# Kernel tuning notes

Measured on AMD Instinct MI355X. Metric: run time of the kernel, lower is better.

Reference implementation:

```python
import jax, jax.numpy as jnp
import numpy as np

B, T, I, H, O = 4096, 256, 16, 32, 1


def setup_inputs() -> dict:
    key = jax.random.key(0)
    ks = jax.random.split(key, 8)
    s_ih = 1.0 / np.sqrt(H)
    x = jax.random.normal(ks[0], (B, T, I), dtype=jnp.float32)
    # PyTorch nn.LSTM params: gate order [i, f, g, o], uniform(-1/sqrt(H), 1/sqrt(H))
    W_ih = jax.random.uniform(ks[1], (4 * H, I), minval=-s_ih, maxval=s_ih, dtype=jnp.float32)
    W_hh = jax.random.uniform(ks[2], (4 * H, H), minval=-s_ih, maxval=s_ih, dtype=jnp.float32)
    b_ih = jax.random.uniform(ks[3], (4 * H,), minval=-s_ih, maxval=s_ih, dtype=jnp.float32)
    b_hh = jax.random.uniform(ks[4], (4 * H,), minval=-s_ih, maxval=s_ih, dtype=jnp.float32)
    W_fc = jax.random.uniform(ks[5], (O, H), minval=-s_ih, maxval=s_ih, dtype=jnp.float32)
    b_fc = jax.random.uniform(ks[6], (O,), minval=-s_ih, maxval=s_ih, dtype=jnp.float32)
    return {"x": x, "W_ih": W_ih, "W_hh": W_hh, "b_ih": b_ih, "b_hh": b_hh,
            "W_fc": W_fc, "b_fc": b_fc}


def _lstm_last_hidden(x, W_ih, W_hh, b_ih, b_hh):
    # Precompute input contributions for all timesteps: [T, B, 4H]
    xg = (jnp.einsum('bti,gi->btg', x, W_ih) + b_ih + b_hh).transpose(1, 0, 2)
    h0 = jnp.zeros((x.shape[0], W_hh.shape[1]), dtype=x.dtype)
    c0 = jnp.zeros_like(h0)

    def step(carry, xg_t):
        h, c = carry
        gates = xg_t + h @ W_hh.T  # [B, 4H]
        i, f, g, o = jnp.split(gates, 4, axis=-1)
        i = jax.nn.sigmoid(i)
        f = jax.nn.sigmoid(f)
        g = jnp.tanh(g)
        o = jax.nn.sigmoid(o)
        c = f * c + i * g
        h = o * jnp.tanh(c)
        return (h, c), None

    (h_last, _), _ = jax.lax.scan(step, (h0, c0), xg)
    return h_last


def reference(x, W_ih, W_hh, b_ih, b_hh, W_fc, b_fc):
    h_last = _lstm_last_hidden(x, W_ih, W_hh, b_ih, b_hh)
    # Dropout is identity in eval mode
    return h_last @ W_fc.T + b_fc  # [B, O]
```

## Files before the change

kernel.cpp:

```cpp
#include <hip/hip_runtime.h>

#define B_ 4096
#define T_ 256
#define I_ 16
#define H_ 32

typedef _Float16 half2_t __attribute__((ext_vector_type(2)));
typedef _Float16 half4_t __attribute__((ext_vector_type(4)));
typedef _Float16 half8_t __attribute__((ext_vector_type(8)));

union H8 {
    half8_t v;
    half2_t h[4];
};

__device__ __forceinline__ float sigm_(float x) {
    float e = __builtin_amdgcn_exp2f(-1.442695041f * x);
    return __builtin_amdgcn_rcpf(1.0f + e);
}
__device__ __forceinline__ float tanh_(float x) {
    float e = __builtin_amdgcn_exp2f(-2.885390082f * x);
    float r = __builtin_amdgcn_rcpf(1.0f + e);
    return __fmaf_rn(2.0f, r, -1.0f);
}

__global__ __launch_bounds__(64, 4)
void lstm_fused_f16(const float* __restrict__ x,
                    const float* __restrict__ Wih,
                    const float* __restrict__ Whh,
                    const float* __restrict__ bih,
                    const float* __restrict__ bhh,
                    const float* __restrict__ Wfc,
                    const float* __restrict__ bfc,
                    float* __restrict__ out)
{
    __shared__ __align__(16) _Float16 hbuf[2][H_];
    __shared__ __align__(16) _Float16 xbuf[2][8 * I_];

    const int tid  = threadIdx.x;
    const int elem = tid >> 5;
    const int idx  = tid & 31;
    const int b    = blockIdx.x * 2 + elem;

    half2_t wih2[4][I_ / 2];
    half2_t whh2[4][H_ / 2];
    float bias[4];
#pragma unroll
    for (int q = 0; q < 4; ++q) {
        const int row = q * 32 + idx;
        const float4* pih = reinterpret_cast<const float4*>(Wih + row * I_);
#pragma unroll
        for (int k = 0; k < I_ / 4; ++k) {
            const float4 v = pih[k];
            wih2[q][2 * k + 0] = half2_t{(_Float16)v.x, (_Float16)v.y};
            wih2[q][2 * k + 1] = half2_t{(_Float16)v.z, (_Float16)v.w};
        }
        const float4* phh = reinterpret_cast<const float4*>(Whh + row * H_);
#pragma unroll
        for (int k = 0; k < H_ / 4; ++k) {
            const float4 v = phh[k];
            whh2[q][2 * k + 0] = half2_t{(_Float16)v.x, (_Float16)v.y};
            whh2[q][2 * k + 1] = half2_t{(_Float16)v.z, (_Float16)v.w};
        }
        bias[q] = bih[row] + bhh[row];
    }

    hbuf[elem][idx] = (_Float16)0.0f;
    float c  = 0.0f;
    float hj = 0.0f;
    __syncthreads();

    const float* xb = x + (size_t)b * (T_ * I_);
    float4 xnext = *reinterpret_cast<const float4*>(xb + idx * 4);

    for (int tb = 0; tb < T_ / 8; ++tb) {
        half4_t xs;
        xs[0] = (_Float16)xnext.x; xs[1] = (_Float16)xnext.y;
        xs[2] = (_Float16)xnext.z; xs[3] = (_Float16)xnext.w;
        *reinterpret_cast<half4_t*>(&xbuf[elem][idx * 4]) = xs;
        if (tb + 1 < T_ / 8) {
            xnext = *reinterpret_cast<const float4*>(xb + (tb + 1) * (8 * I_) + idx * 4);
        }
        __syncthreads();

#pragma unroll
        for (int tt = 0; tt < 8; ++tt) {
            float ai = bias[0], af = bias[1], ag = bias[2], ao = bias[3];

            H8 xv0, xv1;
            xv0.v = *reinterpret_cast<const half8_t*>(&xbuf[elem][tt * I_]);
            xv1.v = *reinterpret_cast<const half8_t*>(&xbuf[elem][tt * I_ + 8]);
#pragma unroll
            for (int k = 0; k < 4; ++k) {
                ai = __builtin_amdgcn_fdot2(xv0.h[k], wih2[0][k], ai, false);
                af = __builtin_amdgcn_fdot2(xv0.h[k], wih2[1][k], af, false);
                ag = __builtin_amdgcn_fdot2(xv0.h[k], wih2[2][k], ag, false);
                ao = __builtin_amdgcn_fdot2(xv0.h[k], wih2[3][k], ao, false);
            }
#pragma unroll
            for (int k = 0; k < 4; ++k) {
                ai = __builtin_amdgcn_fdot2(xv1.h[k], wih2[0][4 + k], ai, false);
                af = __builtin_amdgcn_fdot2(xv1.h[k], wih2[1][4 + k], af, false);
                ag = __builtin_amdgcn_fdot2(xv1.h[k], wih2[2][4 + k], ag, false);
                ao = __builtin_amdgcn_fdot2(xv1.h[k], wih2[3][4 + k], ao, false);
            }

#pragma unroll
            for (int j8 = 0; j8 < 4; ++j8) {
                H8 hv;
                hv.v = *reinterpret_cast<const half8_t*>(&hbuf[elem][j8 * 8]);
#pragma unroll
                for (int k = 0; k < 4; ++k) {
                    const int p = j8 * 4 + k;
                    ai = __builtin_amdgcn_fdot2(hv.h[k], whh2[0][p], ai, false);
                    af = __builtin_amdgcn_fdot2(hv.h[k], whh2[1][p], af, false);
                    ag = __builtin_amdgcn_fdot2(hv.h[k], whh2[2][p], ag, false);
                    ao = __builtin_amdgcn_fdot2(hv.h[k], whh2[3][p], ao, false);
                }
            }

            const float gi = sigm_(ai);
            const float gf = sigm_(af);
            const float gg = tanh_(ag);
            const float go = sigm_(ao);

            c  = __fmaf_rn(gf, c, gi * gg);
            hj = go * tanh_(c);

            hbuf[elem][idx] = (_Float16)hj;
            __syncthreads();
        }
    }

    float p = hj * Wfc[idx];
#pragma unroll
    for (int off = 16; off > 0; off >>= 1) {
        p += __shfl_down(p, off, 32);
    }
    if (idx == 0) {
        out[b] = p + bfc[0];
    }
}

extern "C" void kernel_launch(void* const* d_in, const int* in_sizes, int n_in,
                              void* d_out, int out_size, void* d_ws, size_t ws_size,
                              hipStream_t stream) {
    const float* x   = (const float*)d_in[0];
    const float* Wih = (const float*)d_in[1];
    const float* Whh = (const float*)d_in[2];
    const float* bih = (const float*)d_in[3];
    const float* bhh = (const float*)d_in[4];
    const float* Wfc = (const float*)d_in[5];
    const float* bfc = (const float*)d_in[6];
    float* out = (float*)d_out;

    dim3 grid(B_ / 2);
    dim3 block(64);
    hipLaunchKernelGGL(lstm_fused_f16, grid, block, 0, stream,
                       x, Wih, Whh, bih, bhh, Wfc, bfc, out);
}
```

Before: 239.6 us.

## Split LSTM gates across two half-waves, one batch element per block

Each 64-thread block now handles one batch element instead of two. Each lane computes two gate rows (i/g in the low half, f/o in the high half), and results are exchanged with a cross-half shuffle. This halves the per-step dot-product chain length per lane and uses two accumulators per row for more ILP, which targets the serial recurrence latency. In exchange it doubles the number of blocks, idles half the lanes for the cell update, and doubles the x staging chunk to 16 timesteps.

```diff
diff --git a/kernel.cpp b/kernel.cpp
--- a/kernel.cpp
+++ b/kernel.cpp
@@ -25,119 +25,126 @@
 }
 
 __global__ __launch_bounds__(64, 4)
-void lstm_fused_f16(const float* __restrict__ x,
-                    const float* __restrict__ Wih,
-                    const float* __restrict__ Whh,
-                    const float* __restrict__ bih,
-                    const float* __restrict__ bhh,
-                    const float* __restrict__ Wfc,
-                    const float* __restrict__ bfc,
-                    float* __restrict__ out)
+void lstm_gate_split(const float* __restrict__ x,
+                     const float* __restrict__ Wih,
+                     const float* __restrict__ Whh,
+                     const float* __restrict__ bih,
+                     const float* __restrict__ bhh,
+                     const float* __restrict__ Wfc,
+                     const float* __restrict__ bfc,
+                     float* __restrict__ out)
 {
-    __shared__ __align__(16) _Float16 hbuf[2][H_];
-    __shared__ __align__(16) _Float16 xbuf[2][8 * I_];
+    __shared__ __align__(16) _Float16 hbuf[H_];
+    __shared__ __align__(16) _Float16 xbuf[16 * I_];
 
     const int tid  = threadIdx.x;
-    const int elem = tid >> 5;
-    const int idx  = tid & 31;
-    const int b    = blockIdx.x * 2 + elem;
+    const int b    = blockIdx.x;
+    const bool lo  = (tid < 32);
 
-    half2_t wih2[4][I_ / 2];
-    half2_t whh2[4][H_ / 2];
-    float bias[4];
+    const int rowA = tid;
+    const int rowB = tid + 64;
+
+    half2_t wA[24], wB[24];
 #pragma unroll
-    for (int q = 0; q < 4; ++q) {
-        const int row = q * 32 + idx;
-        const float4* pih = reinterpret_cast<const float4*>(Wih + row * I_);
+    for (int k = 0; k < I_ / 4; ++k) {
+        const float4 va = *reinterpret_cast<const float4*>(Wih + rowA * I_ + 4 * k);
+        wA[2 * k + 0] = half2_t{(_Float16)va.x, (_Float16)va.y};
+        wA[2 * k + 1] = half2_t{(_Float16)va.z, (_Float16)va.w};
+        const float4 vb = *reinterpret_cast<const float4*>(Wih + rowB * I_ + 4 * k);
+        wB[2 * k + 0] = half2_t{(_Float16)vb.x, (_Float16)vb.y};
+        wB[2 * k + 1] = half2_t{(_Float16)vb.z, (_Float16)vb.w};
+    }
 #pragma unroll
-        for (int k = 0; k < I_ / 4; ++k) {
-            const float4 v = pih[k];
-            wih2[q][2 * k + 0] = half2_t{(_Float16)v.x, (_Float16)v.y};
-            wih2[q][2 * k + 1] = half2_t{(_Float16)v.z, (_Float16)v.w};
-        }
-        const float4* phh = reinterpret_cast<const float4*>(Whh + row * H_);
-#pragma unroll
-        for (int k = 0; k < H_ / 4; ++k) {
-            const float4 v = phh[k];
-            whh2[q][2 * k + 0] = half2_t{(_Float16)v.x, (_Float16)v.y};
-            whh2[q][2 * k + 1] = half2_t{(_Float16)v.z, (_Float16)v.w};
-        }
-        bias[q] = bih[row] + bhh[row];
+    for (int k = 0; k < H_ / 4; ++k) {
+        const float4 va = *reinterpret_cast<const float4*>(Whh + rowA * H_ + 4 * k);
+        wA[8 + 2 * k + 0] = half2_t{(_Float16)va.x, (_Float16)va.y};
+        wA[8 + 2 * k + 1] = half2_t{(_Float16)va.z, (_Float16)va.w};
+        const float4 vb = *reinterpret_cast<const float4*>(Whh + rowB * H_ + 4 * k);
+        wB[8 + 2 * k + 0] = half2_t{(_Float16)vb.x, (_Float16)vb.y};
+        wB[8 + 2 * k + 1] = half2_t{(_Float16)vb.z, (_Float16)vb.w};
     }
+    const float biasA = bih[rowA] + bhh[rowA];
+    const float biasB = bih[rowB] + bhh[rowB];
 
-    hbuf[elem][idx] = (_Float16)0.0f;
+    const float mB   = lo ? -2.885390082f : -1.442695041f;
+    const float mulB = lo ? 2.0f : 1.0f;
+    const float addB = lo ? -1.0f : 0.0f;
+
+    if (lo) hbuf[tid] = (_Float16)0.0f;
     float c  = 0.0f;
     float hj = 0.0f;
     __syncthreads();
 
     const float* xb = x + (size_t)b * (T_ * I_);
-    float4 xnext = *reinterpret_cast<const float4*>(xb + idx * 4);
+    float4 xnext = *reinterpret_cast<const float4*>(xb + tid * 4);
 
-    for (int tb = 0; tb < T_ / 8; ++tb) {
+    for (int tb = 0; tb < T_ / 16; ++tb) {
         half4_t xs;
         xs[0] = (_Float16)xnext.x; xs[1] = (_Float16)xnext.y;
         xs[2] = (_Float16)xnext.z; xs[3] = (_Float16)xnext.w;
-        *reinterpret_cast<half4_t*>(&xbuf[elem][idx * 4]) = xs;
-        if (tb + 1 < T_ / 8) {
-            xnext = *reinterpret_cast<const float4*>(xb + (tb + 1) * (8 * I_) + idx * 4);
+        *reinterpret_cast<half4_t*>(&xbuf[tid * 4]) = xs;
+        if (tb + 1 < T_ / 16) {
+            xnext = *reinterpret_cast<const float4*>(xb + (tb + 1) * (16 * I_) + tid * 4);
         }
         __syncthreads();
 
 #pragma unroll
-        for (int tt = 0; tt < 8; ++tt) {
-            float ai = bias[0], af = bias[1], ag = bias[2], ao = bias[3];
+        for (int tt = 0; tt < 16; ++tt) {
+            float aA0 = biasA, aA1 = 0.0f, aB0 = biasB, aB1 = 0.0f;
 
             H8 xv0, xv1;
-            xv0.v = *reinterpret_cast<const half8_t*>(&xbuf[elem][tt * I_]);
-            xv1.v = *reinterpret_cast<const half8_t*>(&xbuf[elem][tt * I_ + 8]);
+            xv0.v = *reinterpret_cast<const half8_t*>(&xbuf[tt * I_]);
+            xv1.v = *reinterpret_cast<const half8_t*>(&xbuf[tt * I_ + 8]);
 #pragma unroll
             for (int k = 0; k < 4; ++k) {
-                ai = __builtin_amdgcn_fdot2(xv0.h[k], wih2[0][k], ai, false);
-                af = __builtin_amdgcn_fdot2(xv0.h[k], wih2[1][k], af, false);
-                ag = __builtin_amdgcn_fdot2(xv0.h[k], wih2[2][k], ag, false);
-                ao = __builtin_amdgcn_fdot2(xv0.h[k], wih2[3][k], ao, false);
+                aA0 = __builtin_amdgcn_fdot2(xv0.h[k], wA[k], aA0, false);
+                aB0 = __builtin_amdgcn_fdot2(xv0.h[k], wB[k], aB0, false);
+                aA1 = __builtin_amdgcn_fdot2(xv1.h[k], wA[4 + k], aA1, false);
+                aB1 = __builtin_amdgcn_fdot2(xv1.h[k], wB[4 + k], aB1, false);
             }
-#pragma unroll
-            for (int k = 0; k < 4; ++k) {
-                ai = __builtin_amdgcn_fdot2(xv1.h[k], wih2[0][4 + k], ai, false);
-                af = __builtin_amdgcn_fdot2(xv1.h[k], wih2[1][4 + k], af, false);
-                ag = __builtin_amdgcn_fdot2(xv1.h[k], wih2[2][4 + k], ag, false);
-                ao = __builtin_amdgcn_fdot2(xv1.h[k], wih2[3][4 + k], ao, false);
-            }
-
 #pragma unroll
             for (int j8 = 0; j8 < 4; ++j8) {
                 H8 hv;
-                hv.v = *reinterpret_cast<const half8_t*>(&hbuf[elem][j8 * 8]);
+                hv.v = *reinterpret_cast<const half8_t*>(&hbuf[j8 * 8]);
 #pragma unroll
                 for (int k = 0; k < 4; ++k) {
-                    const int p = j8 * 4 + k;
-                    ai = __builtin_amdgcn_fdot2(hv.h[k], whh2[0][p], ai, false);
-                    af = __builtin_amdgcn_fdot2(hv.h[k], whh2[1][p], af, false);
-                    ag = __builtin_amdgcn_fdot2(hv.h[k], whh2[2][p], ag, false);
-                    ao = __builtin_amdgcn_fdot2(hv.h[k], whh2[3][p], ao, false);
+                    const int p = 8 + j8 * 4 + k;
+                    if (j8 & 1) {
+                        aA1 = __builtin_amdgcn_fdot2(hv.h[k], wA[p], aA1, false);
+                        aB1 = __builtin_amdgcn_fdot2(hv.h[k], wB[p], aB1, false);
+                    } else {
+                        aA0 = __builtin_amdgcn_fdot2(hv.h[k], wA[p], aA0, false);
+                        aB0 = __builtin_amdgcn_fdot2(hv.h[k], wB[p], aB0, false);
+                    }
                 }
             }
+            const float aA = aA0 + aA1;
+            const float aB = aB0 + aB1;
 
-            const float gi = sigm_(ai);
-            const float gf = sigm_(af);
-            const float gg = tanh_(ag);
-            const float go = sigm_(ao);
+            const float actA = sigm_(aA);
+            const float eB   = __builtin_amdgcn_exp2f(mB * aB);
+            const float sB   = __builtin_amdgcn_rcpf(1.0f + eB);
+            const float actB = __fmaf_rn(mulB, sB, addB);
 
-            c  = __fmaf_rn(gf, c, gi * gg);
-            hj = go * tanh_(c);
+            const float xA = __shfl_xor(actA, 32, 64);
+            const float xB = __shfl_xor(actB, 32, 64);
 
-            hbuf[elem][idx] = (_Float16)hj;
+            if (lo) {
+                c = __fmaf_rn(xA, c, actA * actB);
+                const float tc = tanh_(c);
+                hj = xB * tc;
+                hbuf[tid] = (_Float16)hj;
+            }
             __syncthreads();
         }
     }
 
-    float p = hj * Wfc[idx];
+    float p = lo ? hj * Wfc[tid] : 0.0f;
 #pragma unroll
-    for (int off = 16; off > 0; off >>= 1) {
-        p += __shfl_down(p, off, 32);
+    for (int off = 32; off > 0; off >>= 1) {
+        p += __shfl_down(p, off, 64);
     }
-    if (idx == 0) {
+    if (tid == 0) {
         out[b] = p + bfc[0];
     }
 }
@@ -154,8 +161,8 @@
     const float* bfc = (const float*)d_in[6];
     float* out = (float*)d_out;
 
-    dim3 grid(B_ / 2);
+    dim3 grid(B_);
     dim3 block(64);
-    hipLaunchKernelGGL(lstm_fused_f16, grid, block, 0, stream,
+    hipLaunchKernelGGL(lstm_gate_split, grid, block, 0, stream,
                        x, Wih, Whh, bih, bhh, Wfc, bfc, out);
 }
```

Result: slower. 254.2 us (+6.1%).

## Compute LSTM gates with MFMA over 16 batch elements per block

Applied to the files above, without the earlier changes.

Replaces the per-thread fdot2 gate computation with 16x16x32 f16 MFMA instructions. Each 128-thread block handles 16 sequences, and each wave computes half of the hidden units for all four gates. The input projection becomes a zero-padded MFMA, the bias is pre-scaled and folded into the activation exponent, x is prefetched one 8-step block ahead in registers, and h is double-buffered in LDS. This reduces the ALU work per timestep, but the grid drops to 256 blocks, which may underfill the GPU and leave the serial recurrence latency-bound.

```diff
diff --git a/kernel.cpp b/kernel.cpp
--- a/kernel.cpp
+++ b/kernel.cpp
@@ -5,140 +5,139 @@
 #define I_ 16
 #define H_ 32
 
-typedef _Float16 half2_t __attribute__((ext_vector_type(2)));
-typedef _Float16 half4_t __attribute__((ext_vector_type(4)));
-typedef _Float16 half8_t __attribute__((ext_vector_type(8)));
+typedef _Float16 f16x4 __attribute__((ext_vector_type(4)));
+typedef _Float16 f16x8 __attribute__((ext_vector_type(8)));
+typedef float    f32x4 __attribute__((ext_vector_type(4)));
 
-union H8 {
-    half8_t v;
-    half2_t h[4];
-};
+#define MSIG  (-1.442695041f)
+#define MTANH (-2.885390082f)
 
-__device__ __forceinline__ float sigm_(float x) {
-    float e = __builtin_amdgcn_exp2f(-1.442695041f * x);
-    return __builtin_amdgcn_rcpf(1.0f + e);
-}
-__device__ __forceinline__ float tanh_(float x) {
-    float e = __builtin_amdgcn_exp2f(-2.885390082f * x);
-    float r = __builtin_amdgcn_rcpf(1.0f + e);
-    return __fmaf_rn(2.0f, r, -1.0f);
-}
-
-__global__ __launch_bounds__(64, 4)
-void lstm_fused_f16(const float* __restrict__ x,
-                    const float* __restrict__ Wih,
-                    const float* __restrict__ Whh,
-                    const float* __restrict__ bih,
-                    const float* __restrict__ bhh,
-                    const float* __restrict__ Wfc,
-                    const float* __restrict__ bfc,
-                    float* __restrict__ out)
+__global__ __launch_bounds__(128, 1)
+void lstm_mfma2(const float* __restrict__ x,
+                const float* __restrict__ Wih,
+                const float* __restrict__ Whh,
+                const float* __restrict__ bih,
+                const float* __restrict__ bhh,
+                const float* __restrict__ Wfc,
+                const float* __restrict__ bfc,
+                float* __restrict__ out)
 {
-    __shared__ __align__(16) _Float16 hbuf[2][H_];
-    __shared__ __align__(16) _Float16 xbuf[2][8 * I_];
+    __shared__ __align__(16) _Float16 hbuf[2][16][40];
 
     const int tid  = threadIdx.x;
-    const int elem = tid >> 5;
-    const int idx  = tid & 31;
-    const int b    = blockIdx.x * 2 + elem;
+    const int wave = tid >> 6;
+    const int l    = tid & 63;
+    const int lr   = l & 15;
+    const int lg   = l >> 4;
+    const int b0   = blockIdx.x * 16;
 
-    half2_t wih2[4][I_ / 2];
-    half2_t whh2[4][H_ / 2];
-    float bias[4];
+    f16x8 whhA[4];
+    f16x8 wihA[4];
+    float mb[4][4];
 #pragma unroll
     for (int q = 0; q < 4; ++q) {
-        const int row = q * 32 + idx;
-        const float4* pih = reinterpret_cast<const float4*>(Wih + row * I_);
+        const int rowA = q * 32 + wave * 16 + lr;
+        const float* ph = Whh + rowA * H_ + lg * 8;
 #pragma unroll
-        for (int k = 0; k < I_ / 4; ++k) {
-            const float4 v = pih[k];
-            wih2[q][2 * k + 0] = half2_t{(_Float16)v.x, (_Float16)v.y};
-            wih2[q][2 * k + 1] = half2_t{(_Float16)v.z, (_Float16)v.w};
+        for (int k = 0; k < 8; ++k) whhA[q][k] = (_Float16)ph[k];
+        const float* pi = Wih + rowA * I_ + (lg & 1) * 8;
+#pragma unroll
+        for (int k = 0; k < 8; ++k)
+            wihA[q][k] = (lg < 2) ? (_Float16)pi[k] : (_Float16)0.0f;
+        const float m = (q == 2) ? MTANH : MSIG;
+#pragma unroll
+        for (int r = 0; r < 4; ++r) {
+            const int rowC = q * 32 + wave * 16 + lg * 4 + r;
+            mb[q][r] = m * (bih[rowC] + bhh[rowC]);
         }
-        const float4* phh = reinterpret_cast<const float4*>(Whh + row * H_);
-#pragma unroll
-        for (int k = 0; k < H_ / 4; ++k) {
-            const float4 v = phh[k];
-            whh2[q][2 * k + 0] = half2_t{(_Float16)v.x, (_Float16)v.y};
-            whh2[q][2 * k + 1] = half2_t{(_Float16)v.z, (_Float16)v.w};
-        }
-        bias[q] = bih[row] + bhh[row];
     }
 
-    hbuf[elem][idx] = (_Float16)0.0f;
-    float c  = 0.0f;
-    float hj = 0.0f;
+    for (int i = tid; i < 2 * 16 * 40; i += 128)
+        ((_Float16*)hbuf)[i] = (_Float16)0.0f;
     __syncthreads();
 
-    const float* xb = x + (size_t)b * (T_ * I_);
-    float4 xnext = *reinterpret_cast<const float4*>(xb + idx * 4);
+    float c0 = 0.f, c1 = 0.f, c2 = 0.f, c3 = 0.f;
 
-    for (int tb = 0; tb < T_ / 8; ++tb) {
-        half4_t xs;
-        xs[0] = (_Float16)xnext.x; xs[1] = (_Float16)xnext.y;
-        xs[2] = (_Float16)xnext.z; xs[3] = (_Float16)xnext.w;
-        *reinterpret_cast<half4_t*>(&xbuf[elem][idx * 4]) = xs;
-        if (tb + 1 < T_ / 8) {
-            xnext = *reinterpret_cast<const float4*>(xb + (tb + 1) * (8 * I_) + idx * 4);
-        }
-        __syncthreads();
+    const float* xbase = x + (size_t)(b0 + lr) * (T_ * I_) + (lg & 1) * 8;
+    f16x8 xf[8];
+#pragma unroll
+    for (int k = 0; k < 8; ++k) {
+        const float4 u0 = *reinterpret_cast<const float4*>(xbase + k * I_);
+        const float4 u1 = *reinterpret_cast<const float4*>(xbase + k * I_ + 4);
+        f16x8 w;
+        w[0] = (_Float16)u0.x; w[1] = (_Float16)u0.y;
+        w[2] = (_Float16)u0.z; w[3] = (_Float16)u0.w;
+        w[4] = (_Float16)u1.x; w[5] = (_Float16)u1.y;
+        w[6] = (_Float16)u1.z; w[7] = (_Float16)u1.w;
+        xf[k] = w;
+    }
 
+    const f32x4 zf = {0.f, 0.f, 0.f, 0.f};
+
+    for (int tb = 0; tb < 32; ++tb) {
 #pragma unroll
         for (int tt = 0; tt < 8; ++tt) {
-            float ai = bias[0], af = bias[1], ag = bias[2], ao = bias[3];
-
-            H8 xv0, xv1;
-            xv0.v = *reinterpret_cast<const half8_t*>(&xbuf[elem][tt * I_]);
-            xv1.v = *reinterpret_cast<const half8_t*>(&xbuf[elem][tt * I_ + 8]);
-#pragma unroll
-            for (int k = 0; k < 4; ++k) {
-                ai = __builtin_amdgcn_fdot2(xv0.h[k], wih2[0][k], ai, false);
-                af = __builtin_amdgcn_fdot2(xv0.h[k], wih2[1][k], af, false);
-                ag = __builtin_amdgcn_fdot2(xv0.h[k], wih2[2][k], ag, false);
-                ao = __builtin_amdgcn_fdot2(xv0.h[k], wih2[3][k], ao, false);
-            }
-#pragma unroll
-            for (int k = 0; k < 4; ++k) {
-                ai = __builtin_amdgcn_fdot2(xv1.h[k], wih2[0][4 + k], ai, false);
-                af = __builtin_amdgcn_fdot2(xv1.h[k], wih2[1][4 + k], af, false);
-                ag = __builtin_amdgcn_fdot2(xv1.h[k], wih2[2][4 + k], ag, false);
-                ao = __builtin_amdgcn_fdot2(xv1.h[k], wih2[3][4 + k], ao, false);
+            const f16x8 xB = xf[tt];
+            if (tb < 31) {
+                const float* nx = xbase + ((tb + 1) * 8 + tt) * I_;
+                const float4 u0 = *reinterpret_cast<const float4*>(nx);
+                const float4 u1 = *reinterpret_cast<const float4*>(nx + 4);
+                f16x8 w;
+                w[0] = (_Float16)u0.x; w[1] = (_Float16)u0.y;
+                w[2] = (_Float16)u0.z; w[3] = (_Float16)u0.w;
+                w[4] = (_Float16)u1.x; w[5] = (_Float16)u1.y;
+                w[6] = (_Float16)u1.z; w[7] = (_Float16)u1.w;
+                xf[tt] = w;
             }
 
+            const f16x8 hB = *reinterpret_cast<const f16x8*>(&hbuf[tt & 1][lr][lg * 8]);
+
+            f32x4 a0 = __builtin_amdgcn_mfma_f32_16x16x32_f16(wihA[0], xB, zf, 0, 0, 0);
+            f32x4 a1 = __builtin_amdgcn_mfma_f32_16x16x32_f16(wihA[1], xB, zf, 0, 0, 0);
+            f32x4 a2 = __builtin_amdgcn_mfma_f32_16x16x32_f16(wihA[2], xB, zf, 0, 0, 0);
+            f32x4 a3 = __builtin_amdgcn_mfma_f32_16x16x32_f16(wihA[3], xB, zf, 0, 0, 0);
+            a0 = __builtin_amdgcn_mfma_f32_16x16x32_f16(whhA[0], hB, a0, 0, 0, 0);
+            a1 = __builtin_amdgcn_mfma_f32_16x16x32_f16(whhA[1], hB, a1, 0, 0, 0);
+            a2 = __builtin_amdgcn_mfma_f32_16x16x32_f16(whhA[2], hB, a2, 0, 0, 0);
+            a3 = __builtin_amdgcn_mfma_f32_16x16x32_f16(whhA[3], hB, a3, 0, 0, 0);
+
+            float si[4], sf[4], tg[4], so[4];
 #pragma unroll
-            for (int j8 = 0; j8 < 4; ++j8) {
-                H8 hv;
-                hv.v = *reinterpret_cast<const half8_t*>(&hbuf[elem][j8 * 8]);
-#pragma unroll
-                for (int k = 0; k < 4; ++k) {
-                    const int p = j8 * 4 + k;
-                    ai = __builtin_amdgcn_fdot2(hv.h[k], whh2[0][p], ai, false);
-                    af = __builtin_amdgcn_fdot2(hv.h[k], whh2[1][p], af, false);
-                    ag = __builtin_amdgcn_fdot2(hv.h[k], whh2[2][p], ag, false);
-                    ao = __builtin_amdgcn_fdot2(hv.h[k], whh2[3][p], ao, false);
-                }
+            for (int r = 0; r < 4; ++r) {
+                si[r] = __builtin_amdgcn_rcpf(1.0f + __builtin_amdgcn_exp2f(__fmaf_rn(MSIG,  a0[r], mb[0][r])));
+                sf[r] = __builtin_amdgcn_rcpf(1.0f + __builtin_amdgcn_exp2f(__fmaf_rn(MSIG,  a1[r], mb[1][r])));
+                tg[r] = __fmaf_rn(2.0f, __builtin_amdgcn_rcpf(1.0f + __builtin_amdgcn_exp2f(__fmaf_rn(MTANH, a2[r], mb[2][r]))), -1.0f);
+                so[r] = __builtin_amdgcn_rcpf(1.0f + __builtin_amdgcn_exp2f(__fmaf_rn(MSIG,  a3[r], mb[3][r])));
             }
 
-            const float gi = sigm_(ai);
-            const float gf = sigm_(af);
-            const float gg = tanh_(ag);
-            const float go = sigm_(ao);
+            c0 = __fmaf_rn(sf[0], c0, si[0] * tg[0]);
+            c1 = __fmaf_rn(sf[1], c1, si[1] * tg[1]);
+            c2 = __fmaf_rn(sf[2], c2, si[2] * tg[2]);
+            c3 = __fmaf_rn(sf[3], c3, si[3] * tg[3]);
+            const float t0 = __fmaf_rn(2.0f, __builtin_amdgcn_rcpf(1.0f + __builtin_amdgcn_exp2f(MTANH * c0)), -1.0f);
+            const float t1 = __fmaf_rn(2.0f, __builtin_amdgcn_rcpf(1.0f + __builtin_amdgcn_exp2f(MTANH * c1)), -1.0f);
+            const float t2 = __fmaf_rn(2.0f, __builtin_amdgcn_rcpf(1.0f + __builtin_amdgcn_exp2f(MTANH * c2)), -1.0f);
+            const float t3 = __fmaf_rn(2.0f, __builtin_amdgcn_rcpf(1.0f + __builtin_amdgcn_exp2f(MTANH * c3)), -1.0f);
+            const float h0 = so[0] * t0, h1 = so[1] * t1, h2 = so[2] * t2, h3 = so[3] * t3;
 
-            c  = __fmaf_rn(gf, c, gi * gg);
-            hj = go * tanh_(c);
+            f16x4 hv;
+            hv[0] = (_Float16)h0; hv[1] = (_Float16)h1;
+            hv[2] = (_Float16)h2; hv[3] = (_Float16)h3;
+            *reinterpret_cast<f16x4*>(&hbuf[(tt + 1) & 1][lr][wave * 16 + lg * 4]) = hv;
 
-            hbuf[elem][idx] = (_Float16)hj;
             __syncthreads();
         }
     }
 
-    float p = hj * Wfc[idx];
+    if (tid < 64) {
+        const f16x8 hL = *reinterpret_cast<const f16x8*>(&hbuf[0][lr][lg * 8]);
+        const float* pw = Wfc + lg * 8;
+        float p = 0.f;
 #pragma unroll
-    for (int off = 16; off > 0; off >>= 1) {
-        p += __shfl_down(p, off, 32);
-    }
-    if (idx == 0) {
-        out[b] = p + bfc[0];
+        for (int k = 0; k < 8; ++k) p += (float)hL[k] * pw[k];
+        p += __shfl_xor(p, 16, 64);
+        p += __shfl_xor(p, 32, 64);
+        if (lg == 0) out[b0 + lr] = p + bfc[0];
     }
 }
 
@@ -154,8 +153,8 @@
     const float* bfc = (const float*)d_in[6];
     float* out = (float*)d_out;
 
-    dim3 grid(B_ / 2);
-    dim3 block(64);
-    hipLaunchKernelGGL(lstm_fused_f16, grid, block, 0, stream,
+    dim3 grid(B_ / 16);
+    dim3 block(128);
+    hipLaunchKernelGGL(lstm_mfma2, grid, block, 0, stream,
                        x, Wih, Whh, bih, bhh, Wfc, bfc, out);
 }
```

New measurement: 265.5 us. +10.8%, slower.
